# Kernel tuning notes

Hardware: AMD Instinct MI355X
Metric: run time of the kernel (lower is better)

Reference implementation:

```python
import jax, jax.numpy as jnp
import numpy as np

B, L, D, FF = 4, 4096, 1024, 2048
EPS = 1e-5


def _ln(x, g, b):
    m = jnp.mean(x, axis=-1, keepdims=True)
    v = jnp.var(x, axis=-1, keepdims=True)
    return (x - m) / jnp.sqrt(v + EPS) * g + b


def setup_inputs() -> dict:
    key = jax.random.key(0)
    ks = jax.random.split(key, 9)
    x = jax.random.normal(ks[0], (B, L, D), jnp.float32)
    # phazor init: exp(2j*pi*k/D) * |randn| -> split into re/im float params
    mag = jnp.abs(jax.random.normal(ks[1], (D,), jnp.float32))
    ang = 2.0 * jnp.pi * jnp.arange(D, dtype=jnp.float32) / D
    return dict(
        x=x,
        ln_g=jnp.ones((D,), jnp.float32),
        ln_b=jnp.zeros((D,), jnp.float32),
        fc_w=jax.random.normal(ks[2], (D, D), jnp.float32) * 0.02,
        fc_b=jnp.zeros((D,), jnp.float32),
        w1=jax.random.normal(ks[3], (D, FF), jnp.float32) * 0.02,
        b1=jnp.zeros((FF,), jnp.float32),
        w2=jax.random.normal(ks[4], (FF, D), jnp.float32) * 0.02,
        b2=jnp.zeros((D,), jnp.float32),
        ph_re=mag * jnp.cos(ang),
        ph_im=mag * jnp.sin(ang),
        phi_re=jax.random.normal(ks[5], (D,), jnp.float32),
        phi_im=jax.random.normal(ks[6], (D,), jnp.float32),
        lci_re=jax.random.normal(ks[7], (D,), jnp.float32),
        lci_im=jax.random.normal(ks[8], (D,), jnp.float32),
    )


def _spiral_conv(xn, ph_re, ph_im, phi_re, phi_im, lci_re, lci_im):
    ph = ph_re + 1j * ph_im          # phazor parameter [D]
    phi = phi_re + 1j * phi_im       # phazor_init [D]
    lci = lci_re + 1j * lci_im       # last_conv_init [D]
    a = jnp.abs(ph)
    phz = ph / a * jnp.exp(-a)       # unit direction * decaying magnitude, [D]
    t = jnp.arange(L, dtype=jnp.float32)[:, None]
    prog = jnp.exp(t * jnp.log(phz)[None, :])        # phz**t, [L, D]
    filt = prog * phi[None, :]                       # [L, D]
    filt_fft = jnp.fft.fft(filt, n=2 * L, axis=0)    # [2L, D]
    x_fft = jnp.fft.fft(xn.astype(jnp.complex64), n=2 * L, axis=1)  # [B, 2L, D]
    conv = jnp.fft.ifft(filt_fft[None] * x_fft, axis=1)[:, :L]      # [B, L, D]
    # last_conv is detached in the original (first call uses last_conv_init)
    last = jax.lax.stop_gradient(lci)
    conv = conv + last[None, None, :] * prog[None] * phz[None, None, :]
    return conv.real


def reference(x, ln_g, ln_b, fc_w, fc_b, w1, b1, w2, b2,
              ph_re, ph_im, phi_re, phi_im, lci_re, lci_im):
    xn = _ln(x, ln_g, ln_b)
    c = _spiral_conv(xn, ph_re, ph_im, phi_re, phi_im, lci_re, lci_im)
    y = jax.nn.silu(x @ fc_w + fc_b)
    x2 = c * y + x                  # gated conv + residual (dropout=0 -> identity)
    x3 = _ln(x2, ln_g, ln_b)        # same (shared) LayerNorm instance
    h = jax.nn.silu(x3 @ w1 + b1) @ w2 + b2
    return x2 + h
```

## Files before the change

### kernel.cpp

```cpp
#include <hip/hip_runtime.h>
#include <hip/hip_bf16.h>
#include <hip/hip_fp8.h>
#include <cstdint>
#include <cstddef>

#define B_ 4
#define L_ 4096
#define D_ 1024
#define FF_ 2048
#define ROWS (B_ * L_)
#define EPS_ 1e-5f
#define CG 64
#define CC 64

typedef __attribute__((ext_vector_type(8))) __bf16 bf16x8;
typedef __attribute__((ext_vector_type(4))) float f32x4;
typedef __attribute__((ext_vector_type(4))) unsigned short us4;
typedef __attribute__((ext_vector_type(2))) long l2;

__device__ __forceinline__ float bf2f(unsigned short u) {
  union { unsigned int i; float f; } v; v.i = ((unsigned int)u) << 16; return v.f;
}
__device__ __forceinline__ unsigned short f2bf(float f) {
  union { float f; unsigned int i; } v; v.f = f;
  unsigned int r = v.i + 0x7fffu + ((v.i >> 16) & 1u);
  return (unsigned short)(r >> 16);
}
__device__ __forceinline__ unsigned char f2fp8(float f) {
  __hip_fp8_e4m3 q(f);
  return *reinterpret_cast<unsigned char*>(&q);
}
__device__ __forceinline__ int ph64(int e) {
  return (((e >> 3) & 3) << 4) | (((e >> 5) & 1) << 3) | (e & 7);
}

__global__ __launch_bounds__(256) void transpose_cast(
    const float* __restrict__ in, unsigned short* __restrict__ out, int K, int N) {
  __shared__ float tb[32][33];
  int n0 = blockIdx.x * 32, k0 = blockIdx.y * 32;
  int tx = threadIdx.x & 31, ty = threadIdx.x >> 5;
#pragma unroll
  for (int i = 0; i < 4; ++i) {
    int k = ty + i * 8;
    tb[k][tx] = in[(size_t)(k0 + k) * N + n0 + tx];
  }
  __syncthreads();
#pragma unroll
  for (int i = 0; i < 4; ++i) {
    int n = ty + i * 8;
    out[(size_t)(n0 + n) * K + k0 + tx] = f2bf(tb[tx][n]);
  }
}

__global__ __launch_bounds__(256) void transpose_cast_fp8(
    const float* __restrict__ in, unsigned char* __restrict__ out, int K, int N,
    float scale) {
  __shared__ float tb[32][33];
  int n0 = blockIdx.x * 32, k0 = blockIdx.y * 32;
  int tx = threadIdx.x & 31, ty = threadIdx.x >> 5;
#pragma unroll
  for (int i = 0; i < 4; ++i) {
    int k = ty + i * 8;
    tb[k][tx] = in[(size_t)(k0 + k) * N + n0 + tx];
  }
  __syncthreads();
#pragma unroll
  for (int i = 0; i < 4; ++i) {
    int n = ty + i * 8;
    int k = k0 + tx;
    size_t idx = (size_t)(n0 + n) * K + (k & ~63) + ph64(k & 63);
    out[idx] = f2fp8(tb[tx][n] * scale);
  }
}

__global__ __launch_bounds__(256) void ln1_kernel(
    const float* __restrict__ x, const float* __restrict__ g, const float* __restrict__ b,
    unsigned short* __restrict__ xn, unsigned short* __restrict__ xb) {
  int row = blockIdx.x;
  int t = threadIdx.x;
  const float4* xr = (const float4*)(x + (size_t)row * D_);
  float4 v = xr[t];
  float s = v.x + v.y + v.z + v.w;
  float sq = v.x * v.x + v.y * v.y + v.z * v.z + v.w * v.w;
#pragma unroll
  for (int off = 32; off > 0; off >>= 1) {
    s += __shfl_down(s, off);
    sq += __shfl_down(sq, off);
  }
  __shared__ float ls[4], lq[4];
  int lane = t & 63, w = t >> 6;
  if (lane == 0) { ls[w] = s; lq[w] = sq; }
  __syncthreads();
  s = ls[0] + ls[1] + ls[2] + ls[3];
  sq = lq[0] + lq[1] + lq[2] + lq[3];
  float mean = s * (1.0f / D_);
  float var = sq * (1.0f / D_) - mean * mean;
  float rstd = rsqrtf(var + EPS_);
  float4 gv = ((const float4*)g)[t];
  float4 bv = ((const float4*)b)[t];
  us4 o, ob;
  o.x = f2bf((v.x - mean) * rstd * gv.x + bv.x);
  o.y = f2bf((v.y - mean) * rstd * gv.y + bv.y);
  o.z = f2bf((v.z - mean) * rstd * gv.z + bv.z);
  o.w = f2bf((v.w - mean) * rstd * gv.w + bv.w);
  ob.x = f2bf(v.x); ob.y = f2bf(v.y); ob.z = f2bf(v.z); ob.w = f2bf(v.w);
  ((us4*)(xn + (size_t)row * D_))[t] = o;
  ((us4*)(xb + (size_t)row * D_))[t] = ob;
}

__global__ __launch_bounds__(256) void conv_pass1(
    const unsigned short* __restrict__ xn, const float* __restrict__ ph_re,
    const float* __restrict__ ph_im, float2* __restrict__ rloc) {
  int d = blockIdx.x * 256 + threadIdx.x;
  int g = blockIdx.y, b = blockIdx.z;
  float re = ph_re[d], im = ph_im[d];
  float a = sqrtf(re * re + im * im);
  float sc = expf(-a) / a;
  float pr = re * sc, pi = im * sc;
  float rr = 0.f, ri = 0.f;
  const unsigned short* xp = xn + ((size_t)(b * L_ + g * CC)) * D_ + d;
#pragma unroll 8
  for (int l = 0; l < CC; ++l) {
    float xv = bf2f(xp[(size_t)l * D_]);
    float nr = pr * rr - pi * ri + xv;
    ri = pr * ri + pi * rr;
    rr = nr;
  }
  rloc[((size_t)(b * CG + g)) * D_ + d] = make_float2(rr, ri);
}

__global__ __launch_bounds__(256) void conv_pass2(
    const float* __restrict__ ph_re, const float* __restrict__ ph_im,
    const float2* __restrict__ rloc, float2* __restrict__ carry) {
  int idx = blockIdx.x * 256 + threadIdx.x;
  int b = idx >> 10, d = idx & (D_ - 1);
  float re = ph_re[d], im = ph_im[d];
  float a = sqrtf(re * re + im * im);
  float th = atan2f(im, re);
  float rho = expf(-a * (float)CC);
  float ang = th * (float)CC;
  float pcr = rho * cosf(ang), pci = rho * sinf(ang);
  float cr = 0.f, ci = 0.f;
  for (int g0 = 0; g0 < CG; g0 += 8) {
    float2 rl[8];
    float2 cw[8];
#pragma unroll
    for (int i = 0; i < 8; ++i)
      rl[i] = rloc[((size_t)(b * CG + g0 + i)) * D_ + d];
#pragma unroll
    for (int i = 0; i < 8; ++i) {
      cw[i] = make_float2(cr, ci);
      float nr = pcr * cr - pci * ci + rl[i].x;
      ci = pcr * ci + pci * cr + rl[i].y;
      cr = nr;
    }
#pragma unroll
    for (int i = 0; i < 8; ++i)
      carry[((size_t)(b * CG + g0 + i)) * D_ + d] = cw[i];
  }
}

__global__ __launch_bounds__(256) void conv_pass3(
    const unsigned short* __restrict__ xn,
    const float* __restrict__ ph_re, const float* __restrict__ ph_im,
    const float* __restrict__ phi_re, const float* __restrict__ phi_im,
    const float* __restrict__ lci_re, const float* __restrict__ lci_im,
    const float2* __restrict__ carry, unsigned short* __restrict__ cout) {
  int d = blockIdx.x * 256 + threadIdx.x;
  int g = blockIdx.y, b = blockIdx.z;
  float re = ph_re[d], im = ph_im[d];
  float a = sqrtf(re * re + im * im);
  float sc = expf(-a) / a;
  float pr = re * sc, pi = im * sc;
  float th = atan2f(im, re);
  int l0 = g * CC;
  float rho = expf(-a * (float)(l0 + 1));
  float ang = th * (float)(l0 + 1);
  float prr = rho * cosf(ang), pri = rho * sinf(ang);
  float fr = phi_re[d], fi = phi_im[d];
  float qr = lci_re[d], qi = lci_im[d];
  float2 cv = carry[((size_t)(b * CG + g)) * D_ + d];
  float rr = cv.x, ri = cv.y;
  const unsigned short* xp = xn + ((size_t)(b * L_ + l0)) * D_ + d;
  unsigned short* cp = cout + ((size_t)(b * L_ + l0)) * D_ + d;
#pragma unroll 4
  for (int l = 0; l < CC; ++l) {
    float xv = bf2f(xp[(size_t)l * D_]);
    float nr = pr * rr - pi * ri + xv;
    ri = pr * ri + pi * rr;
    rr = nr;
    float outv = fr * rr - fi * ri + qr * prr - qi * pri;
    cp[(size_t)l * D_] = f2bf(outv);
    float pn = pr * prr - pi * pri;
    pri = pr * pri + pi * prr;
    prr = pn;
  }
}

__global__ __launch_bounds__(256) void ln2c_kernel(
    const unsigned short* __restrict__ x2, const float* __restrict__ g,
    const float* __restrict__ b, unsigned char* __restrict__ x3) {
  int row = blockIdx.x;
  int t = threadIdx.x;
  size_t base = (size_t)row * D_;
  us4 vb = ((const us4*)(x2 + base))[t];
  float4 v;
  v.x = bf2f(vb.x); v.y = bf2f(vb.y); v.z = bf2f(vb.z); v.w = bf2f(vb.w);
  float s = v.x + v.y + v.z + v.w;
  float sq = v.x * v.x + v.y * v.y + v.z * v.z + v.w * v.w;
#pragma unroll
  for (int off = 32; off > 0; off >>= 1) {
    s += __shfl_down(s, off);
    sq += __shfl_down(sq, off);
  }
  __shared__ float ls[4], lq[4];
  int lane = t & 63, w = t >> 6;
  if (lane == 0) { ls[w] = s; lq[w] = sq; }
  __syncthreads();
  s = ls[0] + ls[1] + ls[2] + ls[3];
  sq = lq[0] + lq[1] + lq[2] + lq[3];
  float mean = s * (1.0f / D_);
  float var = sq * (1.0f / D_) - mean * mean;
  float rstd = rsqrtf(var + EPS_);
  float4 gv = ((const float4*)g)[t];
  float4 bv = ((const float4*)b)[t];
  uchar4 o;
  o.x = f2fp8((v.x - mean) * rstd * gv.x + bv.x);
  o.y = f2fp8((v.y - mean) * rstd * gv.y + bv.y);
  o.z = f2fp8((v.z - mean) * rstd * gv.z + bv.z);
  o.w = f2fp8((v.w - mean) * rstd * gv.w + bv.w);
  int d = t * 4;
  size_t idx = base + (size_t)((d & ~63) + ph64(d & 63));
  *((uchar4*)(x3 + idx)) = o;
}

__device__ __forceinline__ void gld_lds16(const void* gp, void* lp) {
  __builtin_amdgcn_global_load_lds(
      (const __attribute__((address_space(1))) unsigned int*)gp,
      (__attribute__((address_space(3))) unsigned int*)lp, 16, 0, 0);
}

__global__ __launch_bounds__(512, 4) void gemm_bt_gate(
    const unsigned short* __restrict__ A, const unsigned short* __restrict__ Bt,
    const float* __restrict__ bias,
    const unsigned short* __restrict__ gate, const unsigned short* __restrict__ xresb,
    unsigned short* __restrict__ Cv, int NB, int GROUP, int N, int K) {
  __shared__ unsigned short As[3][256 * 32];
  __shared__ unsigned short Bs[3][128 * 32];

  int nwg = gridDim.x;
  int xcd = blockIdx.x & 7;
  int lo = blockIdx.x >> 3;
  int q = nwg >> 3;
  int gsz = GROUP * NB;
  int g_ = lo / gsz, r_ = lo % gsz;
  int n_ = r_ / GROUP, ml = r_ - n_ * GROUP;
  int Mx = q / NB;
  int bm0 = (xcd * Mx + g_ * GROUP + ml) * 256;
  int bn0 = n_ * 128;

  int t = threadIdx.x;
  int lane = t & 63, w = t >> 6;
  int wr = w >> 1, wc = w & 1;
  int frr = lane & 15, cl = lane >> 4;
  int sw = (frr >> 1) & 3;
  int rA0 = wr * 64 + frr;
  int rB0 = wc * 64 + frr;
  int ko = (cl ^ sw) * 8;

  int nt = K >> 5;

  int tr = t >> 2;
  int jc = (t & 3) ^ ((tr >> 1) & 3);
  const unsigned short* pA = A + (size_t)(bm0 + tr) * K + jc * 8;
  const unsigned short* pB = Bt + (size_t)(bn0 + tr) * K + jc * 8;

  auto stA = [&](int kt2, int slot, int c) {
    gld_lds16(pA + (size_t)kt2 * 32 + (size_t)c * 128 * K, &As[slot][c * 4096 + t * 8]);
  };
  auto stB = [&](int kt2, int slot) {
    gld_lds16(pB + (size_t)kt2 * 32, &Bs[slot][t * 8]);
  };

  f32x4 acc[4][4] = {};

  stA(0, 0, 0); stA(0, 0, 1); stB(0, 0);
  stA(1, 1, 0); stA(1, 1, 1); stB(1, 1);
  asm volatile("s_waitcnt vmcnt(3)" ::: "memory");
  __builtin_amdgcn_s_barrier();

  int s = 0;
  for (int kt = 0; kt < nt; ++kt) {
    const unsigned short* as = As[s];
    const unsigned short* bs = Bs[s];
    int s2 = s + 2; if (s2 >= 3) s2 -= 3;
    bool p2 = kt + 2 < nt;

    bf16x8 av[4], bv[4];
#pragma unroll
    for (int m = 0; m < 4; ++m) av[m] = *(const bf16x8*)&as[(rA0 + m * 16) * 32 + ko];
#pragma unroll
    for (int n = 0; n < 4; ++n) bv[n] = *(const bf16x8*)&bs[(rB0 + n * 16) * 32 + ko];
    if (p2) { stA(kt + 2, s2, 0); stA(kt + 2, s2, 1); stB(kt + 2, s2); }

    asm volatile("s_waitcnt lgkmcnt(0)" ::: "memory");
    __builtin_amdgcn_sched_barrier(0);
    __builtin_amdgcn_s_setprio(1);
#pragma unroll
    for (int m = 0; m < 4; ++m)
#pragma unroll
      for (int n = 0; n < 4; ++n)
        acc[m][n] = __builtin_amdgcn_mfma_f32_16x16x32_bf16(av[m], bv[n], acc[m][n], 0, 0, 0);
    __builtin_amdgcn_s_setprio(0);

    if (p2) { asm volatile("s_waitcnt vmcnt(3)" ::: "memory"); }
    else    { asm volatile("s_waitcnt vmcnt(0)" ::: "memory"); }
    __builtin_amdgcn_s_barrier();
    s += 1; if (s == 3) s = 0;
  }

#pragma unroll
  for (int m = 0; m < 4; ++m) {
#pragma unroll
    for (int n = 0; n < 4; ++n) {
#pragma unroll
      for (int r = 0; r < 4; ++r) {
        int row = bm0 + wr * 64 + m * 16 + cl * 4 + r;
        int col = bn0 + wc * 64 + n * 16 + frr;
        size_t o = (size_t)row * N + col;
        float v = acc[m][n][r] + bias[col];
        v = v / (1.0f + __expf(-v));
        v = bf2f(gate[o]) * v + bf2f(xresb[o]);
        Cv[o] = f2bf(v);
      }
    }
  }
}

template <int SILU, int RESBF, int OUT_FP8>
__global__ __launch_bounds__(512, 4) void gemm_f8(
    const unsigned char* __restrict__ A, const unsigned char* __restrict__ Bt,
    const float* __restrict__ bias, const unsigned short* __restrict__ resb,
    float oscale, void* __restrict__ Cv, int NB, int GROUP, int N, int K) {
  __shared__ unsigned char As[3][256 * 64];
  __shared__ unsigned char Bs[3][128 * 64];

  int nwg = gridDim.x;
  int xcd = blockIdx.x & 7;
  int lo = blockIdx.x >> 3;
  int q = nwg >> 3;
  int gsz = GROUP * NB;
  int g_ = lo / gsz, r_ = lo % gsz;
  int n_ = r_ / GROUP, ml = r_ - n_ * GROUP;
  int Mx = q / NB;
  int bm0 = (xcd * Mx + g_ * GROUP + ml) * 256;
  int bn0 = n_ * 128;

  int t = threadIdx.x;
  int lane = t & 63, w = t >> 6;
  int wr = w >> 1, wc = w & 1;
  int frr = lane & 15, cl = lane >> 4;
  int sw = (frr >> 1) & 3;
  int rA0 = wr * 64 + frr;
  int rB0 = wc * 64 + frr;
  int ko = (cl ^ sw) * 16;

  int nt = K >> 6;

  int tr = t >> 2;
  int jc = (t & 3) ^ ((tr >> 1) & 3);
  const unsigned char* pA = A + (size_t)(bm0 + tr) * K + jc * 16;
  const unsigned char* pB = Bt + (size_t)(bn0 + tr) * K + jc * 16;

  auto stA = [&](int kt2, int slot, int c) {
    gld_lds16(pA + (size_t)kt2 * 64 + (size_t)c * 128 * K, &As[slot][c * 8192 + t * 16]);
  };
  auto stB = [&](int kt2, int slot) {
    gld_lds16(pB + (size_t)kt2 * 64, &Bs[slot][t * 16]);
  };

  f32x4 acc[4][4] = {};

  stA(0, 0, 0); stA(0, 0, 1); stB(0, 0);
  stA(1, 1, 0); stA(1, 1, 1); stB(1, 1);
  asm volatile("s_waitcnt vmcnt(3)" ::: "memory");
  __builtin_amdgcn_s_barrier();

  int s = 0;
  for (int kt = 0; kt < nt; ++kt) {
    const unsigned char* as = As[s];
    const unsigned char* bs = Bs[s];
    int s2 = s + 2; if (s2 >= 3) s2 -= 3;
    bool p2 = kt + 2 < nt;

    l2 av[4], bv[4];
#pragma unroll
    for (int m = 0; m < 4; ++m) av[m] = *(const l2*)&as[(rA0 + m * 16) * 64 + ko];
#pragma unroll
    for (int n = 0; n < 4; ++n) bv[n] = *(const l2*)&bs[(rB0 + n * 16) * 64 + ko];
    if (p2) { stA(kt + 2, s2, 0); stA(kt + 2, s2, 1); stB(kt + 2, s2); }

    asm volatile("s_waitcnt lgkmcnt(0)" ::: "memory");
    __builtin_amdgcn_sched_barrier(0);
    __builtin_amdgcn_s_setprio(1);
#pragma unroll
    for (int m = 0; m < 4; ++m)
#pragma unroll
      for (int n = 0; n < 4; ++n)
        acc[m][n] = __builtin_amdgcn_mfma_f32_16x16x32_fp8_fp8(av[m].x, bv[n].x, acc[m][n], 0, 0, 0);
#pragma unroll
    for (int m = 0; m < 4; ++m)
#pragma unroll
      for (int n = 0; n < 4; ++n)
        acc[m][n] = __builtin_amdgcn_mfma_f32_16x16x32_fp8_fp8(av[m].y, bv[n].y, acc[m][n], 0, 0, 0);
    __builtin_amdgcn_s_setprio(0);

    if (p2) { asm volatile("s_waitcnt vmcnt(3)" ::: "memory"); }
    else    { asm volatile("s_waitcnt vmcnt(0)" ::: "memory"); }
    __builtin_amdgcn_s_barrier();
    s += 1; if (s == 3) s = 0;
  }

#pragma unroll
  for (int m = 0; m < 4; ++m) {
#pragma unroll
    for (int n = 0; n < 4; ++n) {
#pragma unroll
      for (int r = 0; r < 4; ++r) {
        int row = bm0 + wr * 64 + m * 16 + cl * 4 + r;
        int col = bn0 + wc * 64 + n * 16 + frr;
        size_t o = (size_t)row * N + col;
        float v = acc[m][n][r] * oscale + bias[col];
        if (SILU) v = v / (1.0f + __expf(-v));
        if (RESBF) v += bf2f(resb[o]);
        if (OUT_FP8) {
          int e = n * 16 + frr;
          size_t op = (size_t)row * N + bn0 + wc * 64 + ph64(e);
          ((unsigned char*)Cv)[op] = f2fp8(v);
        } else {
          ((float*)Cv)[o] = v;
        }
      }
    }
  }
}

extern "C" void kernel_launch(void* const* d_in, const int* in_sizes, int n_in,
                              void* d_out, int out_size, void* d_ws, size_t ws_size,
                              hipStream_t stream) {
  const float* x      = (const float*)d_in[0];
  const float* ln_g   = (const float*)d_in[1];
  const float* ln_b   = (const float*)d_in[2];
  const float* fc_w   = (const float*)d_in[3];
  const float* fc_b   = (const float*)d_in[4];
  const float* w1     = (const float*)d_in[5];
  const float* b1     = (const float*)d_in[6];
  const float* w2     = (const float*)d_in[7];
  const float* b2     = (const float*)d_in[8];
  const float* ph_re  = (const float*)d_in[9];
  const float* ph_im  = (const float*)d_in[10];
  const float* phi_re = (const float*)d_in[11];
  const float* phi_im = (const float*)d_in[12];
  const float* lci_re = (const float*)d_in[13];
  const float* lci_im = (const float*)d_in[14];
  float* out = (float*)d_out;

  char* ws = (char*)d_ws;
  const size_t SZ_BF = (size_t)ROWS * D_ * 2;
  const size_t SZ_F8 = (size_t)ROWS * D_;
  unsigned short* xn_x2 = (unsigned short*)(ws);
  unsigned short* cbuf  = (unsigned short*)(ws + SZ_BF);
  unsigned short* xb    = (unsigned short*)(ws + 2 * SZ_BF);
  unsigned char*  x3f8  = (unsigned char*)(ws + 3 * SZ_BF);
  unsigned char*  h1f8  = (unsigned char*)(ws + 3 * SZ_BF + SZ_F8);
  char* wp = ws + 3 * SZ_BF + SZ_F8 + (size_t)ROWS * FF_;
  unsigned short* fc_wt = (unsigned short*)(wp);
  unsigned char*  w1t8  = (unsigned char*)(wp + (size_t)D_ * D_ * 2);
  unsigned char*  w2t8  = (unsigned char*)(wp + (size_t)D_ * D_ * 2 + (size_t)D_ * FF_);
  float2* rloc  = (float2*)(wp + (size_t)D_ * D_ * 2 + 2 * (size_t)D_ * FF_);
  float2* carry = rloc + (size_t)B_ * CG * D_;

  transpose_cast<<<dim3(D_ / 32, D_ / 32), 256, 0, stream>>>(fc_w, fc_wt, D_, D_);
  transpose_cast_fp8<<<dim3(FF_ / 32, D_ / 32), 256, 0, stream>>>(w1, w1t8, D_, FF_, 32.0f);
  transpose_cast_fp8<<<dim3(D_ / 32, FF_ / 32), 256, 0, stream>>>(w2, w2t8, FF_, D_, 32.0f);

  ln1_kernel<<<ROWS, 256, 0, stream>>>(x, ln_g, ln_b, xn_x2, xb);

  conv_pass1<<<dim3(D_ / 256, CG, B_), 256, 0, stream>>>(xn_x2, ph_re, ph_im, rloc);
  conv_pass2<<<dim3((B_ * D_) / 256), 256, 0, stream>>>(ph_re, ph_im, rloc, carry);
  conv_pass3<<<dim3(D_ / 256, CG, B_), 256, 0, stream>>>(xn_x2, ph_re, ph_im, phi_re, phi_im,
                                                         lci_re, lci_im, carry, cbuf);

  gemm_bt_gate<<<(ROWS / 256) * (D_ / 128), 512, 0, stream>>>(
      xb, fc_wt, fc_b, cbuf, xb, xn_x2, D_ / 128, 4, D_, D_);

  ln2c_kernel<<<ROWS, 256, 0, stream>>>(xn_x2, ln_g, ln_b, x3f8);

  gemm_f8<1, 0, 1><<<(ROWS / 256) * (FF_ / 128), 512, 0, stream>>>(
      x3f8, w1t8, b1, nullptr, 1.0f / 32.0f, h1f8, FF_ / 128, 4, FF_, D_);

  gemm_f8<0, 1, 0><<<(ROWS / 256) * (D_ / 128), 512, 0, stream>>>(
      h1f8, w2t8, b2, xn_x2, 1.0f / 32.0f, out, D_ / 128, 2, D_, FF_);
}
```

Measured before the change: 247.9 us.

## Switch FP8 GEMM to 32x32x64 scaled MFMA with natural K layout

```diff
diff --git a/kernel.cpp b/kernel.cpp
--- a/kernel.cpp
+++ b/kernel.cpp
@@ -15,8 +15,16 @@
 
 typedef __attribute__((ext_vector_type(8))) __bf16 bf16x8;
 typedef __attribute__((ext_vector_type(4))) float f32x4;
+typedef __attribute__((ext_vector_type(16))) float f32x16;
 typedef __attribute__((ext_vector_type(4))) unsigned short us4;
-typedef __attribute__((ext_vector_type(2))) long l2;
+typedef __attribute__((ext_vector_type(4))) int i32x4;
+typedef __attribute__((ext_vector_type(8))) int i32x8;
+
+#if __has_builtin(__builtin_amdgcn_mfma_scale_f32_32x32x64_f8f6f4)
+#define HAS_MX 1
+#else
+#define HAS_MX 0
+#endif
 
 __device__ __forceinline__ float bf2f(unsigned short u) {
   union { unsigned int i; float f; } v; v.i = ((unsigned int)u) << 16; return v.f;
@@ -29,9 +37,6 @@
 __device__ __forceinline__ unsigned char f2fp8(float f) {
   __hip_fp8_e4m3 q(f);
   return *reinterpret_cast<unsigned char*>(&q);
-}
-__device__ __forceinline__ int ph64(int e) {
-  return (((e >> 3) & 3) << 4) | (((e >> 5) & 1) << 3) | (e & 7);
 }
 
 __global__ __launch_bounds__(256) void transpose_cast(
@@ -67,9 +72,7 @@
 #pragma unroll
   for (int i = 0; i < 4; ++i) {
     int n = ty + i * 8;
-    int k = k0 + tx;
-    size_t idx = (size_t)(n0 + n) * K + (k & ~63) + ph64(k & 63);
-    out[idx] = f2fp8(tb[tx][n] * scale);
+    out[(size_t)(n0 + n) * K + k0 + tx] = f2fp8(tb[tx][n] * scale);
   }
 }
 
@@ -229,9 +232,7 @@
   o.y = f2fp8((v.y - mean) * rstd * gv.y + bv.y);
   o.z = f2fp8((v.z - mean) * rstd * gv.z + bv.z);
   o.w = f2fp8((v.w - mean) * rstd * gv.w + bv.w);
-  int d = t * 4;
-  size_t idx = base + (size_t)((d & ~63) + ph64(d & 63));
-  *((uchar4*)(x3 + idx)) = o;
+  ((uchar4*)(x3 + base))[t] = o;
 }
 
 __device__ __forceinline__ void gld_lds16(const void* gp, void* lp) {
@@ -359,11 +360,6 @@
   int t = threadIdx.x;
   int lane = t & 63, w = t >> 6;
   int wr = w >> 1, wc = w & 1;
-  int frr = lane & 15, cl = lane >> 4;
-  int sw = (frr >> 1) & 3;
-  int rA0 = wr * 64 + frr;
-  int rB0 = wc * 64 + frr;
-  int ko = (cl ^ sw) * 16;
 
   int nt = K >> 6;
 
@@ -379,7 +375,17 @@
     gld_lds16(pB + (size_t)kt2 * 64, &Bs[slot][t * 16]);
   };
 
+#if HAS_MX
+  int l31 = lane & 31, h = lane >> 5;
+  int rA0 = wr * 64 + l31;
+  int rB0 = wc * 64 + l31;
+  f32x16 acc[2][2] = {};
+#else
+  int frr = lane & 15, cl = lane >> 4;
+  int rA0 = wr * 64 + frr;
+  int rB0 = wc * 64 + frr;
   f32x4 acc[4][4] = {};
+#endif
 
   stA(0, 0, 0); stA(0, 0, 1); stB(0, 0);
   stA(1, 1, 0); stA(1, 1, 1); stB(1, 1);
@@ -393,27 +399,73 @@
     int s2 = s + 2; if (s2 >= 3) s2 -= 3;
     bool p2 = kt + 2 < nt;
 
-    l2 av[4], bv[4];
-#pragma unroll
-    for (int m = 0; m < 4; ++m) av[m] = *(const l2*)&as[(rA0 + m * 16) * 64 + ko];
-#pragma unroll
-    for (int n = 0; n < 4; ++n) bv[n] = *(const l2*)&bs[(rB0 + n * 16) * 64 + ko];
+#if HAS_MX
+    i32x8 av[2], bv[2];
+#pragma unroll
+    for (int mi = 0; mi < 2; ++mi) {
+      int r = rA0 + mi * 32;
+      int swr = (r >> 1) & 3;
+      const unsigned char* bp = &as[r * 64];
+      i32x4 lo4 = *(const i32x4*)&bp[((2 * h) ^ swr) * 16];
+      i32x4 hi4 = *(const i32x4*)&bp[((2 * h + 1) ^ swr) * 16];
+      av[mi] = __builtin_shufflevector(lo4, hi4, 0, 1, 2, 3, 4, 5, 6, 7);
+    }
+#pragma unroll
+    for (int ni = 0; ni < 2; ++ni) {
+      int r = rB0 + ni * 32;
+      int swr = (r >> 1) & 3;
+      const unsigned char* bp = &bs[r * 64];
+      i32x4 lo4 = *(const i32x4*)&bp[((2 * h) ^ swr) * 16];
+      i32x4 hi4 = *(const i32x4*)&bp[((2 * h + 1) ^ swr) * 16];
+      bv[ni] = __builtin_shufflevector(lo4, hi4, 0, 1, 2, 3, 4, 5, 6, 7);
+    }
     if (p2) { stA(kt + 2, s2, 0); stA(kt + 2, s2, 1); stB(kt + 2, s2); }
 
     asm volatile("s_waitcnt lgkmcnt(0)" ::: "memory");
     __builtin_amdgcn_sched_barrier(0);
     __builtin_amdgcn_s_setprio(1);
 #pragma unroll
+    for (int mi = 0; mi < 2; ++mi)
+#pragma unroll
+      for (int ni = 0; ni < 2; ++ni)
+        acc[mi][ni] = __builtin_amdgcn_mfma_scale_f32_32x32x64_f8f6f4(
+            av[mi], bv[ni], acc[mi][ni], 0, 0, 0, 0x7F, 0, 0x7F);
+    __builtin_amdgcn_s_setprio(0);
+#else
+    long a0[4], b0[4], a1[4], b1[4];
+#pragma unroll
+    for (int m = 0; m < 4; ++m) {
+      int r = rA0 + m * 16;
+      int swr = (r >> 1) & 3;
+      const unsigned char* bp = &as[r * 64];
+      a0[m] = *(const long*)&bp[((cl >> 1) ^ swr) * 16 + (cl & 1) * 8];
+      a1[m] = *(const long*)&bp[(((cl + 4) >> 1) ^ swr) * 16 + (cl & 1) * 8];
+    }
+#pragma unroll
+    for (int n = 0; n < 4; ++n) {
+      int r = rB0 + n * 16;
+      int swr = (r >> 1) & 3;
+      const unsigned char* bp = &bs[r * 64];
+      b0[n] = *(const long*)&bp[((cl >> 1) ^ swr) * 16 + (cl & 1) * 8];
+      b1[n] = *(const long*)&bp[(((cl + 4) >> 1) ^ swr) * 16 + (cl & 1) * 8];
+    }
+    if (p2) { stA(kt + 2, s2, 0); stA(kt + 2, s2, 1); stB(kt + 2, s2); }
+
+    asm volatile("s_waitcnt lgkmcnt(0)" ::: "memory");
+    __builtin_amdgcn_sched_barrier(0);
+    __builtin_amdgcn_s_setprio(1);
+#pragma unroll
     for (int m = 0; m < 4; ++m)
 #pragma unroll
       for (int n = 0; n < 4; ++n)
-        acc[m][n] = __builtin_amdgcn_mfma_f32_16x16x32_fp8_fp8(av[m].x, bv[n].x, acc[m][n], 0, 0, 0);
+        acc[m][n] = __builtin_amdgcn_mfma_f32_16x16x32_fp8_fp8(a0[m], b0[n], acc[m][n], 0, 0, 0);
 #pragma unroll
     for (int m = 0; m < 4; ++m)
 #pragma unroll
       for (int n = 0; n < 4; ++n)
-        acc[m][n] = __builtin_amdgcn_mfma_f32_16x16x32_fp8_fp8(av[m].y, bv[n].y, acc[m][n], 0, 0, 0);
+        acc[m][n] = __builtin_amdgcn_mfma_f32_16x16x32_fp8_fp8(a1[m], b1[n], acc[m][n], 0, 0, 0);
     __builtin_amdgcn_s_setprio(0);
+#endif
 
     if (p2) { asm volatile("s_waitcnt vmcnt(3)" ::: "memory"); }
     else    { asm volatile("s_waitcnt vmcnt(0)" ::: "memory"); }
@@ -421,6 +473,25 @@
     s += 1; if (s == 3) s = 0;
   }
 
+#if HAS_MX
+#pragma unroll
+  for (int mi = 0; mi < 2; ++mi) {
+#pragma unroll
+    for (int ni = 0; ni < 2; ++ni) {
+#pragma unroll
+      for (int rg = 0; rg < 16; ++rg) {
+        int row = bm0 + wr * 64 + mi * 32 + (rg & 3) + 8 * (rg >> 2) + 4 * h;
+        int col = bn0 + wc * 64 + ni * 32 + l31;
+        size_t o = (size_t)row * N + col;
+        float v = acc[mi][ni][rg] * oscale + bias[col];
+        if (SILU) v = v / (1.0f + __expf(-v));
+        if (RESBF) v += bf2f(resb[o]);
+        if (OUT_FP8) ((unsigned char*)Cv)[o] = f2fp8(v);
+        else         ((float*)Cv)[o] = v;
+      }
+    }
+  }
+#else
 #pragma unroll
   for (int m = 0; m < 4; ++m) {
 #pragma unroll
@@ -433,16 +504,12 @@
         float v = acc[m][n][r] * oscale + bias[col];
         if (SILU) v = v / (1.0f + __expf(-v));
         if (RESBF) v += bf2f(resb[o]);
-        if (OUT_FP8) {
-          int e = n * 16 + frr;
-          size_t op = (size_t)row * N + bn0 + wc * 64 + ph64(e);
-          ((unsigned char*)Cv)[op] = f2fp8(v);
-        } else {
-          ((float*)Cv)[o] = v;
-        }
+        if (OUT_FP8) ((unsigned char*)Cv)[o] = f2fp8(v);
+        else         ((float*)Cv)[o] = v;
       }
     }
   }
+#endif
 }
 
 extern "C" void kernel_launch(void* const* d_in, const int* in_sizes, int n_in,
```

New measurement: 234.1 us. 5.6% less time.
